# Performance work log

Hardware: AMD Instinct MI355X
Metric: run time of the kernel (lower is better)

## Reference

```python
import jax, jax.numpy as jnp
import numpy as np

D_MODEL = 1024
N_HEADS = 16
D_HEAD = D_MODEL // N_HEADS
EPS = 1e-6


def setup_inputs() -> dict:
    key = jax.random.key(0)
    ks = jax.random.split(key, 11)
    N, L, S = 4, 4096, 4096
    scale = 1.0 / np.sqrt(D_MODEL)
    inp = {
        "queries": jax.random.normal(ks[0], (N, L, D_MODEL), jnp.float32),
        "keys": jax.random.normal(ks[1], (N, S, D_MODEL), jnp.float32),
        "values": jax.random.normal(ks[2], (N, S, D_MODEL), jnp.float32),
        "Wq": jax.random.normal(ks[3], (D_MODEL, D_MODEL), jnp.float32) * scale,
        "bq": jnp.zeros((D_MODEL,), jnp.float32),
        "Wk": jax.random.normal(ks[4], (D_MODEL, D_MODEL), jnp.float32) * scale,
        "bk": jnp.zeros((D_MODEL,), jnp.float32),
        "Wv": jax.random.normal(ks[5], (D_MODEL, D_MODEL), jnp.float32) * scale,
        "bv": jnp.zeros((D_MODEL,), jnp.float32),
        "Wo": jax.random.normal(ks[6], (D_MODEL, D_MODEL), jnp.float32) * scale,
        "bo": jnp.zeros((D_MODEL,), jnp.float32),
    }
    return inp


def reference(queries, keys, values, Wq, bq, Wk, bk, Wv, bv, Wo, bo):
    N, L, _ = queries.shape
    S = keys.shape[1]
    H, Dh = N_HEADS, D_HEAD
    # projections (torch Linear: x @ W.T + b)
    q = (queries @ Wq.T + bq).reshape(N, L, H, Dh)
    k = (keys @ Wk.T + bk).reshape(N, S, H, Dh)
    v = (values @ Wv.T + bv).reshape(N, S, H, Dh)
    # elu+1 feature map
    Q = jax.nn.elu(q) + 1.0
    K = jax.nn.elu(k) + 1.0
    # KV summary: [N,H,Dv,Dh]
    KV = jnp.einsum('nshd,nshm->nhmd', K, v)
    # normalizer: [N,L,H]
    Z = 1.0 / (jnp.einsum('nlhd,nhd->nlh', Q, K.sum(axis=1)) + EPS)
    # output per head: [N,L,H,Dv]
    V = jnp.einsum('nlhd,nhmd,nlh->nlhm', Q, KV, Z)
    out = V.reshape(N, L, H * Dh) @ Wo.T + bo
    return out
```

## Files before the change

kernel.cpp:

```cpp
#include <hip/hip_runtime.h>
#include <hip/hip_bf16.h>

typedef __attribute__((ext_vector_type(8))) short short8;
typedef __attribute__((ext_vector_type(4))) short short4v;
typedef __attribute__((ext_vector_type(4))) float f32x4;

#define MFMA16(a, b, c) __builtin_amdgcn_mfma_f32_16x16x32_bf16(a, b, c, 0, 0, 0)

__device__ __forceinline__ unsigned short f2bf(float f) {
    unsigned int u = __float_as_uint(f);
    unsigned int r = u + 0x7fffu + ((u >> 16) & 1u);
    return (unsigned short)(r >> 16);
}
__device__ __forceinline__ float bf2f(unsigned short h) {
    return __uint_as_float(((unsigned int)h) << 16);
}
__device__ __forceinline__ unsigned int pk2(float lo, float hi) {
    return (unsigned int)f2bf(lo) | ((unsigned int)f2bf(hi) << 16);
}
__device__ __forceinline__ unsigned int cvtpk(float lo, float hi) {
    unsigned int r;
    asm("v_cvt_pk_bf16_f32 %0, %1, %2" : "=v"(r) : "v"(lo), "v"(hi));
    return r;
}

__device__ __forceinline__ void async16(const void* g, void* l) {
    __builtin_amdgcn_global_load_lds(
        (const __attribute__((address_space(1))) unsigned int*)g,
        (__attribute__((address_space(3))) unsigned int*)l, 16, 0, 0);
}

#define S_BARRIER() asm volatile("s_barrier" ::: "memory")
#define SCHED_FENCE() __builtin_amdgcn_sched_barrier(0)

__global__ __launch_bounds__(256) void cvt4_kernel(const float* __restrict__ w0,
                                                   const float* __restrict__ w1,
                                                   const float* __restrict__ w2,
                                                   const float* __restrict__ w3,
                                                   unsigned short* __restrict__ o0,
                                                   unsigned short* __restrict__ o1,
                                                   unsigned short* __restrict__ o2,
                                                   unsigned short* __restrict__ o3) {
    int wsel = blockIdx.x >> 7;
    int lb = blockIdx.x & 127;
    const float* in = wsel == 0 ? w0 : wsel == 1 ? w1 : wsel == 2 ? w2 : w3;
    unsigned short* out = wsel == 0 ? o0 : wsel == 1 ? o1 : wsel == 2 ? o2 : o3;
    for (int i = lb * 256 + threadIdx.x; i < 131072; i += 32768) {
        float4 v0 = reinterpret_cast<const float4*>(in)[2 * i];
        float4 v1 = reinterpret_cast<const float4*>(in)[2 * i + 1];
        uint4 p;
        p.x = pk2(v0.x, v0.y); p.y = pk2(v0.z, v0.w);
        p.z = pk2(v1.x, v1.y); p.w = pk2(v1.z, v1.w);
        reinterpret_cast<uint4*>(out)[i] = p;
    }
}

__device__ __forceinline__ void gemm_f32a(const float* __restrict__ A,
                                          const unsigned short* __restrict__ B,
                                          const float* __restrict__ bias,
                                          void* __restrict__ out,
                                          int mode, char* lds, int bid) {
    const int tid = threadIdx.x;
    const int lane = tid & 63, wid = tid >> 6;
    const int wr = wid >> 2, wc = wid & 3;
    const int lr = lane & 15, lg = lane >> 4;

    const int swz = (bid & 7) * 32 + (bid >> 3);
    const int bm = swz >> 2, bn = swz & 3;
    const long row0 = (long)bm * 256;
    const long col0 = (long)bn * 256;

    const float* srcA[4];
#pragma unroll
    for (int g = 0; g < 4; ++g) {
        int s = g * 512 + tid;
        int pr = s >> 3;
        int dc = (s & 7) ^ (pr & 7);
        srcA[g] = A + (row0 + pr) * 1024 + dc * 4;
    }
    const unsigned short* srcB[2];
#pragma unroll
    for (int g = 0; g < 2; ++g) {
        int s = g * 512 + tid;
        int pr = s >> 3;
        int dc = (s & 7) ^ (pr & 7);
        srcB[g] = B + (col0 + pr + 128 * (dc >> 2)) * 1024 + (dc & 3) * 8;
    }
    const int dst = tid * 16;

#define STAGE_A(BUF, KT) do {                                                   \
        async16(srcA[0] + (KT) * 32, (BUF) + dst);                              \
        async16(srcA[1] + (KT) * 32, (BUF) + 8192 + dst);                       \
        async16(srcA[2] + (KT) * 32, (BUF) + 16384 + dst);                      \
        async16(srcA[3] + (KT) * 32, (BUF) + 24576 + dst); } while (0)
#define STAGE_B(BUF, KT) do {                                                   \
        async16(srcB[0] + (KT) * 32, (BUF) + 32768 + dst);                      \
        async16(srcB[1] + (KT) * 32, (BUF) + 40960 + dst); } while (0)

    int offA[8];
#pragma unroll
    for (int m = 0; m < 8; ++m)
        offA[m] = (wr * 128 + m * 16 + lr) * 128 + (((2 * lg) ^ (lr & 7)) << 4);
    int offB[4];
#pragma unroll
    for (int n = 0; n < 4; ++n)
        offB[n] = 32768 + ((wc & 1) * 64 + n * 16 + lr) * 128 +
                  ((((wc >> 1) * 4 + lg) ^ (lr & 7)) << 4);

    f32x4 acc[8][4] = {};

    char* p0 = lds;
    char* p1 = lds + 49152;
    char* p2 = lds + 98304;

    STAGE_A(p0, 0); STAGE_B(p0, 0);
    STAGE_A(p1, 1); STAGE_B(p1, 1);
    asm volatile("s_waitcnt vmcnt(6)" ::: "memory");
    SCHED_FENCE();
    S_BARRIER();

#pragma unroll 1
    for (int kt = 0; kt < 32; ++kt) {
        short8 b[4];
        {
            float4 a0[4], a1[4];
#pragma unroll
            for (int m = 0; m < 4; ++m) {
                a0[m] = *(const float4*)(p0 + offA[m]);
                a1[m] = *(const float4*)(p0 + (offA[m] ^ 16));
            }
#pragma unroll
            for (int n = 0; n < 4; ++n) b[n] = *(const short8*)(p0 + offB[n]);
            SCHED_FENCE();
            if (kt < 30) STAGE_A(p2, kt + 2);
            asm volatile("s_waitcnt lgkmcnt(0)" ::: "memory");
            SCHED_FENCE();
            short8 af[4];
#pragma unroll
            for (int m = 0; m < 4; ++m) {
                union { unsigned int u[4]; short8 s; } cv;
                cv.u[0] = cvtpk(a0[m].x, a0[m].y);
                cv.u[1] = cvtpk(a0[m].z, a0[m].w);
                cv.u[2] = cvtpk(a1[m].x, a1[m].y);
                cv.u[3] = cvtpk(a1[m].z, a1[m].w);
                af[m] = cv.s;
            }
            __builtin_amdgcn_s_setprio(1);
#pragma unroll
            for (int m = 0; m < 4; ++m)
#pragma unroll
                for (int n = 0; n < 4; ++n)
                    acc[m][n] = MFMA16(af[m], b[n], acc[m][n]);
            __builtin_amdgcn_s_setprio(0);
            SCHED_FENCE();
            S_BARRIER();
        }
        {
            float4 a0[4], a1[4];
#pragma unroll
            for (int m = 0; m < 4; ++m) {
                a0[m] = *(const float4*)(p0 + offA[4 + m]);
                a1[m] = *(const float4*)(p0 + (offA[4 + m] ^ 16));
            }
            SCHED_FENCE();
            if (kt < 30) STAGE_B(p2, kt + 2);
            if (kt < 30) {
                asm volatile("s_waitcnt vmcnt(6)" ::: "memory");
            } else {
                asm volatile("s_waitcnt vmcnt(0)" ::: "memory");
            }
            SCHED_FENCE();
            asm volatile("s_waitcnt lgkmcnt(0)" ::: "memory");
            SCHED_FENCE();
            short8 af[4];
#pragma unroll
            for (int m = 0; m < 4; ++m) {
                union { unsigned int u[4]; short8 s; } cv;
                cv.u[0] = cvtpk(a0[m].x, a0[m].y);
                cv.u[1] = cvtpk(a0[m].z, a0[m].w);
                cv.u[2] = cvtpk(a1[m].x, a1[m].y);
                cv.u[3] = cvtpk(a1[m].z, a1[m].w);
                af[m] = cv.s;
            }
            __builtin_amdgcn_s_setprio(1);
#pragma unroll
            for (int m = 0; m < 4; ++m)
#pragma unroll
                for (int n = 0; n < 4; ++n)
                    acc[4 + m][n] = MFMA16(af[m], b[n], acc[4 + m][n]);
            __builtin_amdgcn_s_setprio(0);
            SCHED_FENCE();
            S_BARRIER();
        }
        char* t_ = p0; p0 = p1; p1 = p2; p2 = t_;
    }
#undef STAGE_A
#undef STAGE_B

    const int r4 = lg * 4;
    if (mode == 0) {
        char* ep = lds + wid * 4608;
#pragma unroll
        for (int m = 0; m < 8; ++m) {
#pragma unroll
            for (int n = 0; n < 4; ++n) {
                float bcol = bias[col0 + wc * 64 + n * 16 + lr];
#pragma unroll
                for (int j = 0; j < 4; ++j) {
                    float v = acc[m][n][j] + bcol;
                    v = v > 0.f ? v + 1.f : __expf(v);
                    *(float*)(ep + (((lg * 4 + j) * 68) + n * 16 + lr) * 4) = v;
                }
            }
            asm volatile("s_waitcnt lgkmcnt(0)" ::: "memory");
            SCHED_FENCE();
            long R0b = row0 + wr * 128 + m * 16;
            unsigned short* O = (unsigned short*)out;
#pragma unroll
            for (int i = 0; i < 2; ++i) {
                int r = i * 8 + (lane >> 3), c8 = (lane & 7) * 8;
                float4 u0 = *(const float4*)(ep + (r * 68 + c8) * 4);
                float4 u1 = *(const float4*)(ep + (r * 68 + c8 + 4) * 4);
                uint4 w;
                w.x = pk2(u0.x, u0.y); w.y = pk2(u0.z, u0.w);
                w.z = pk2(u1.x, u1.y); w.w = pk2(u1.z, u1.w);
                *(uint4*)(O + (R0b + r) * 1024 + col0 + wc * 64 + c8) = w;
            }
            asm volatile("s_waitcnt lgkmcnt(0)" ::: "memory");
            SCHED_FENCE();
        }
    } else {
#pragma unroll
        for (int m = 0; m < 8; ++m) {
#pragma unroll
            for (int n = 0; n < 4; ++n) {
                long col = col0 + wc * 64 + n * 16 + lr;
                float bcol = bias[col];
                long R0 = row0 + wr * 128 + m * 16 + r4;
                unsigned short* O = (unsigned short*)out;
                long nb = R0 >> 12;
                long s = R0 & 4095;
                short4v pack;
#pragma unroll
                for (int j = 0; j < 4; ++j) {
                    float v = acc[m][n][j] + bcol;
                    if (mode == 1) v = v > 0.f ? v + 1.f : __expf(v);
                    pack[j] = (short)f2bf(v);
                }
                *(short4v*)(O + ((nb << 10) + col) * 4096 + s) = pack;
            }
        }
    }
}

__device__ __forceinline__ void gemm_body(const unsigned short* __restrict__ A,
                                          const unsigned short* __restrict__ B,
                                          const float* __restrict__ bias,
                                          float* __restrict__ out,
                                          char* lds, int bid) {
    const int tid = threadIdx.x;
    const int lane = tid & 63, wid = tid >> 6;
    const int wr = wid >> 2, wc = wid & 3;
    const int lr = lane & 15, lg = lane >> 4;

    const int swz = (bid & 7) * 32 + (bid >> 3);
    const int bm = swz >> 2, bn = swz & 3;
    const long row0 = (long)bm * 256;
    const long col0 = (long)bn * 256;

    const unsigned short* srcA[2];
    const unsigned short* srcB[2];
    int dstOff[2];
#pragma unroll
    for (int g = 0; g < 2; ++g) {
        int s = g * 512 + tid;
        int pr = s >> 3;
        int dc = (s & 7) ^ (pr & 7);
        srcA[g] = A + (row0 + (pr & 63) + 128 * (pr >> 6)) * 1024 + dc * 8;
        srcB[g] = B + (col0 + pr) * 1024 + dc * 8;
        dstOff[g] = s * 16;
    }

#define STG_AQ(BB, Q, KT) do {                                                  \
        async16(srcA[0] + (Q) * 65536 + (KT) * 64,                              \
                lds + (BB) * 65536 + (Q) * 16384 + dstOff[0]);                  \
        async16(srcA[1] + (Q) * 65536 + (KT) * 64,                              \
                lds + (BB) * 65536 + (Q) * 16384 + dstOff[1]); } while (0)
#define STG_BH(BB, H, KT) do {                                                  \
        async16(srcB[0] + (H) * 131072 + (KT) * 64,                             \
                lds + (BB) * 65536 + 32768 + (H) * 16384 + dstOff[0]);          \
        async16(srcB[1] + (H) * 131072 + (KT) * 64,                             \
                lds + (BB) * 65536 + 32768 + (H) * 16384 + dstOff[1]); } while (0)

    const int ch0 = ((lg ^ (lr & 7)) << 4);
    const int ch1 = (((4 + lg) ^ (lr & 7)) << 4);
    const int aB0 = (64 * wr + lr) * 128 + ch0;
    const int aB1 = (64 * wr + lr) * 128 + ch1;
    const int bB0 = 32768 + (wc >> 1) * 16384 + ((wc & 1) * 64 + lr) * 128 + ch0;
    const int bB1 = 32768 + (wc >> 1) * 16384 + ((wc & 1) * 64 + lr) * 128 + ch1;

    f32x4 acc[8][4] = {};
    short8 b0[4], b1[4];

#define GATE4() do { asm volatile("s_waitcnt vmcnt(4)" ::: "memory"); SCHED_FENCE(); } while (0)
#define GATE0() do { asm volatile("s_waitcnt vmcnt(0)" ::: "memory"); SCHED_FENCE(); } while (0)
#define MFMA_BLOCK(MB, BV) do {                                                 \
        S_BARRIER();                                                            \
        asm volatile("s_waitcnt lgkmcnt(0)" ::: "memory");                      \
        SCHED_FENCE();                                                          \
        __builtin_amdgcn_s_setprio(1);                                          \
        _Pragma("unroll") for (int m = 0; m < 4; ++m)                           \
            _Pragma("unroll") for (int n = 0; n < 4; ++n)                       \
                acc[(MB) + m][n] = MFMA16(a[m], BV[n], acc[(MB) + m][n]);       \
        __builtin_amdgcn_s_setprio(0);                                          \
        SCHED_FENCE();                                                          \
        S_BARRIER(); } while (0)
#define LOAD_A(BUFB, ABASE, Q) do {                                             \
        _Pragma("unroll") for (int m = 0; m < 4; ++m)                           \
            a[m] = *(const short8*)(lds + (BUFB) + (Q) * 16384 + (ABASE) + m * 2048); } while (0)
#define LOAD_B(BUFB, BBASE, BV) do {                                            \
        _Pragma("unroll") for (int n = 0; n < 4; ++n)                           \
            BV[n] = *(const short8*)(lds + (BUFB) + (BBASE) + n * 2048); } while (0)

    STG_AQ(0, 0, 0); STG_BH(0, 0, 0); STG_BH(0, 1, 0); STG_AQ(0, 1, 0);
    STG_AQ(1, 0, 1); STG_BH(1, 0, 1);
    GATE4();
    S_BARRIER();

#pragma unroll 1
    for (int t = 0; t < 7; ++t) {
        const int ktA = 2 * t + 1, ktB = 2 * t + 2, ktC = 2 * t + 3;
        { short8 a[4]; LOAD_B(0, bB0, b0); LOAD_A(0, aB0, 0); STG_BH(1, 1, ktA); MFMA_BLOCK(0, b0); }
        { short8 a[4]; LOAD_B(0, bB1, b1); LOAD_A(0, aB1, 0); STG_AQ(1, 1, ktA); MFMA_BLOCK(0, b1); }
        { short8 a[4]; LOAD_A(0, aB0, 1); STG_AQ(0, 0, ktB); MFMA_BLOCK(4, b0); }
        { short8 a[4]; LOAD_A(0, aB1, 1); STG_BH(0, 0, ktB); GATE4(); MFMA_BLOCK(4, b1); }
        { short8 a[4]; LOAD_B(65536, bB0, b0); LOAD_A(65536, aB0, 0); STG_BH(0, 1, ktB); MFMA_BLOCK(0, b0); }
        { short8 a[4]; LOAD_B(65536, bB1, b1); LOAD_A(65536, aB1, 0); STG_AQ(0, 1, ktB); MFMA_BLOCK(0, b1); }
        { short8 a[4]; LOAD_A(65536, aB0, 1); STG_AQ(1, 0, ktC); MFMA_BLOCK(4, b0); }
        { short8 a[4]; LOAD_A(65536, aB1, 1); STG_BH(1, 0, ktC); GATE4(); MFMA_BLOCK(4, b1); }
    }
    {
        { short8 a[4]; LOAD_B(0, bB0, b0); LOAD_A(0, aB0, 0); STG_BH(1, 1, 15); MFMA_BLOCK(0, b0); }
        { short8 a[4]; LOAD_B(0, bB1, b1); LOAD_A(0, aB1, 0); STG_AQ(1, 1, 15); MFMA_BLOCK(0, b1); }
        { short8 a[4]; LOAD_A(0, aB0, 1); MFMA_BLOCK(4, b0); }
        { short8 a[4]; LOAD_A(0, aB1, 1); GATE0(); MFMA_BLOCK(4, b1); }
        { short8 a[4]; LOAD_B(65536, bB0, b0); LOAD_A(65536, aB0, 0); MFMA_BLOCK(0, b0); }
        { short8 a[4]; LOAD_B(65536, bB1, b1); LOAD_A(65536, aB1, 0); MFMA_BLOCK(0, b1); }
        { short8 a[4]; LOAD_A(65536, aB0, 1); MFMA_BLOCK(4, b0); }
        { short8 a[4]; LOAD_A(65536, aB1, 1); MFMA_BLOCK(4, b1); }
    }
#undef STG_AQ
#undef STG_BH
#undef GATE4
#undef GATE0
#undef MFMA_BLOCK
#undef LOAD_A
#undef LOAD_B

    {
        char* ep = lds + wid * 4608;
#pragma unroll
        for (int m = 0; m < 8; ++m) {
#pragma unroll
            for (int n = 0; n < 4; ++n) {
                float bcol = bias[col0 + wc * 64 + n * 16 + lr];
#pragma unroll
                for (int j = 0; j < 4; ++j)
                    *(float*)(ep + (((lg * 4 + j) * 68) + n * 16 + lr) * 4) = acc[m][n][j] + bcol;
            }
            asm volatile("s_waitcnt lgkmcnt(0)" ::: "memory");
            SCHED_FENCE();
            long R0b = row0 + wr * 128 + m * 16;
#pragma unroll
            for (int i = 0; i < 4; ++i) {
                int r = i * 4 + (lane >> 4), c4 = (lane & 15) * 4;
                float4 u = *(const float4*)(ep + (r * 68 + c4) * 4);
                *(float4*)(out + (R0b + r) * 1024 + col0 + wc * 64 + c4) = u;
            }
            asm volatile("s_waitcnt lgkmcnt(0)" ::: "memory");
            SCHED_FENCE();
        }
    }
}

__global__ __launch_bounds__(512, 1) void proj_gemm(const float* __restrict__ q,
                                                    const float* __restrict__ k,
                                                    const float* __restrict__ v,
                                                    const unsigned short* __restrict__ Wqb,
                                                    const unsigned short* __restrict__ Wkb,
                                                    const unsigned short* __restrict__ Wvb,
                                                    const float* __restrict__ bq,
                                                    const float* __restrict__ bk,
                                                    const float* __restrict__ bv,
                                                    unsigned short* __restrict__ Qm,
                                                    unsigned short* __restrict__ Kt,
                                                    unsigned short* __restrict__ vT) {
    __shared__ __align__(16) char lds[147456];
    int seg = blockIdx.x >> 8;
    int bid = blockIdx.x & 255;
    const float* A = seg == 0 ? q : seg == 1 ? k : v;
    const unsigned short* B = seg == 0 ? Wqb : seg == 1 ? Wkb : Wvb;
    const float* bias = seg == 0 ? bq : seg == 1 ? bk : bv;
    void* out = seg == 0 ? (void*)Qm : seg == 1 ? (void*)Kt : (void*)vT;
    gemm_f32a(A, B, bias, out, seg, lds, bid);
}

__global__ __launch_bounds__(512, 1) void out_gemm(const unsigned short* __restrict__ Vbuf,
                                                   const unsigned short* __restrict__ Wob,
                                                   const float* __restrict__ bo,
                                                   float* __restrict__ out) {
    __shared__ __align__(16) char lds[131072];
    gemm_body(Vbuf, Wob, bo, out, lds, blockIdx.x);
}

__global__ __launch_bounds__(256) void kv_kernel(const unsigned short* __restrict__ Kt,
                                                 const unsigned short* __restrict__ vT,
                                                 float* __restrict__ KV,
                                                 float* __restrict__ Ksum) {
    int b = blockIdx.x;
    int sc = b & 7, h = (b >> 3) & 15, n = b >> 7;
    const int tid = threadIdx.x, lane = tid & 63, wave = tid >> 6;
    long base = ((long)(n * 1024 + h * 64)) * 4096 + sc * 512;
    const unsigned short* Kp = Kt + base;
    const unsigned short* Vp = vT + base;
    const int lr = lane & 15, lk = (lane >> 4) * 8;

    f32x4 acc[4] = {};
    float ksa[4] = {0.f, 0.f, 0.f, 0.f};
    for (int s0 = 0; s0 < 512; s0 += 32) {
        short8 a = *(const short8*)(Vp + (long)(wave * 16 + lr) * 4096 + s0 + lk);
#pragma unroll
        for (int d4 = 0; d4 < 4; ++d4) {
            short8 bb = *(const short8*)(Kp + (long)(d4 * 16 + lr) * 4096 + s0 + lk);
            acc[d4] = MFMA16(a, bb, acc[d4]);
            if (wave == 0) {
                float t = 0.f;
#pragma unroll
                for (int e = 0; e < 8; ++e) t += bf2f((unsigned short)bb[e]);
                ksa[d4] += t;
            }
        }
    }
    float* KVb = KV + (long)(n * 16 + h) * 4096;
#pragma unroll
    for (int d4 = 0; d4 < 4; ++d4)
#pragma unroll
        for (int j = 0; j < 4; ++j) {
            int m = wave * 16 + (lane >> 4) * 4 + j;
            int d = d4 * 16 + lr;
            atomicAdd(KVb + m * 64 + d, acc[d4][j]);
        }
    if (wave == 0) {
#pragma unroll
        for (int d4 = 0; d4 < 4; ++d4) {
            float t = ksa[d4];
            t += __shfl_xor(t, 16, 64);
            t += __shfl_xor(t, 32, 64);
            if (lane < 16) atomicAdd(Ksum + n * 1024 + h * 64 + d4 * 16 + lane, t);
        }
    }
}

__global__ __launch_bounds__(256) void attn_kernel(const unsigned short* __restrict__ Qm,
                                                   const float* __restrict__ KV,
                                                   const float* __restrict__ Ksum,
                                                   unsigned short* __restrict__ Vbuf) {
    __shared__ unsigned short Qs[128 * 64];
    __shared__ unsigned short KVs[64 * 64];
    __shared__ float zin[128];
    __shared__ float ks[64];
    int b = blockIdx.x;
    int lc = b & 31, h = (b >> 5) & 15, n = b >> 9;
    int tid = threadIdx.x, lane = tid & 63, wave = tid >> 6;
    long l0 = (long)n * 4096 + lc * 128;

    const unsigned short* Qg = Qm + (l0 + (tid >> 3)) * 1024 + h * 64 + (tid & 7) * 8;
    char* QsB = (char*)Qs + (wave << 10);
#pragma unroll
    for (int it = 0; it < 4; ++it)
        async16(Qg + (long)it * 32 * 1024, QsB + it * 4096);

    const float* kvp = KV + (long)(n * 16 + h) * 4096;
    for (int i = tid * 4; i < 4096; i += 1024) {
        float4 v = *reinterpret_cast<const float4*>(kvp + i);
        short4v p;
        p[0] = (short)f2bf(v.x); p[1] = (short)f2bf(v.y);
        p[2] = (short)f2bf(v.z); p[3] = (short)f2bf(v.w);
        *(short4v*)(KVs + i) = p;
    }
    if (tid < 64) ks[tid] = Ksum[n * 1024 + h * 64 + tid];
    __syncthreads();

    {
        int row = tid >> 1, half = tid & 1;
        float den = 0.f;
        const unsigned short* qrow = Qs + row * 64 + half * 32;
#pragma unroll
        for (int d = 0; d < 32; ++d) den += bf2f(qrow[d]) * ks[half * 32 + d];
        den += __shfl_xor(den, 1, 64);
        if (half == 0) zin[row] = 1.0f / (den + 1e-6f);
    }
    __syncthreads();

    const int lr = lane & 15, lk = (lane >> 4) * 8;
    f32x4 acc[2][4] = {};
#pragma unroll
    for (int kk = 0; kk < 2; ++kk) {
        short8 a0 = *(const short8*)(Qs + (wave * 32 + lr) * 64 + kk * 32 + lk);
        short8 a1 = *(const short8*)(Qs + (wave * 32 + 16 + lr) * 64 + kk * 32 + lk);
#pragma unroll
        for (int nn = 0; nn < 4; ++nn) {
            short8 bb = *(const short8*)(KVs + (nn * 16 + lr) * 64 + kk * 32 + lk);
            acc[0][nn] = MFMA16(a0, bb, acc[0][nn]);
            acc[1][nn] = MFMA16(a1, bb, acc[1][nn]);
        }
    }

    {
        char* ep = (char*)Qs + wave * 4096;
#pragma unroll
        for (int mi = 0; mi < 2; ++mi) {
#pragma unroll
            for (int nn = 0; nn < 4; ++nn)
#pragma unroll
                for (int j = 0; j < 4; ++j) {
                    int rloc = (lane >> 4) * 4 + j;
                    float v = acc[mi][nn][j] * zin[wave * 32 + mi * 16 + rloc];
                    *(float*)(ep + (rloc * 64 + nn * 16 + lr) * 4) = v;
                }
            asm volatile("s_waitcnt lgkmcnt(0)" ::: "memory");
            SCHED_FENCE();
#pragma unroll
            for (int i = 0; i < 2; ++i) {
                int r = i * 8 + (lane >> 3), c8 = (lane & 7) * 8;
                float4 u0 = *(const float4*)(ep + (r * 64 + c8) * 4);
                float4 u1 = *(const float4*)(ep + (r * 64 + c8 + 4) * 4);
                uint4 w;
                w.x = pk2(u0.x, u0.y); w.y = pk2(u0.z, u0.w);
                w.z = pk2(u1.x, u1.y); w.w = pk2(u1.z, u1.w);
                *(uint4*)(Vbuf + (l0 + wave * 32 + mi * 16 + r) * 1024 + h * 64 + c8) = w;
            }
            asm volatile("s_waitcnt lgkmcnt(0)" ::: "memory");
            SCHED_FENCE();
        }
    }
}

extern "C" void kernel_launch(void* const* d_in, const int* in_sizes, int n_in,
                              void* d_out, int out_size, void* d_ws, size_t ws_size,
                              hipStream_t stream) {
    const float* queries = (const float*)d_in[0];
    const float* keys    = (const float*)d_in[1];
    const float* values  = (const float*)d_in[2];
    const float* Wq = (const float*)d_in[3];
    const float* bq = (const float*)d_in[4];
    const float* Wk = (const float*)d_in[5];
    const float* bk = (const float*)d_in[6];
    const float* Wv = (const float*)d_in[7];
    const float* bv = (const float*)d_in[8];
    const float* Wo = (const float*)d_in[9];
    const float* bo = (const float*)d_in[10];
    float* out = (float*)d_out;

    char* ws = (char*)d_ws;
    const size_t SZ = (size_t)16384 * 1024 * 2;
    const size_t WSZ = (size_t)1024 * 1024 * 2;
    unsigned short* Wqb = (unsigned short*)(ws);
    unsigned short* Wkb = (unsigned short*)(ws + WSZ);
    unsigned short* Wvb = (unsigned short*)(ws + 2 * WSZ);
    unsigned short* Wob = (unsigned short*)(ws + 3 * WSZ);
    unsigned short* Qm   = (unsigned short*)(ws + 4 * WSZ);
    unsigned short* Kt   = (unsigned short*)(ws + 4 * WSZ + SZ);
    unsigned short* vT   = (unsigned short*)(ws + 4 * WSZ + 2 * SZ);
    unsigned short* Vbuf = (unsigned short*)(ws + 4 * WSZ + 3 * SZ);
    float* KVf = (float*)(ws + 4 * WSZ + 4 * SZ);
    float* Ksf = (float*)(ws + 4 * WSZ + 4 * SZ + 1048576);

    hipMemsetAsync(KVf, 0, 1048576 + 16384, stream);

    cvt4_kernel<<<512, 256, 0, stream>>>(Wq, Wk, Wv, Wo, Wqb, Wkb, Wvb, Wob);

    proj_gemm<<<768, 512, 0, stream>>>(queries, keys, values, Wqb, Wkb, Wvb,
                                       bq, bk, bv, Qm, Kt, vT);

    kv_kernel<<<512, 256, 0, stream>>>(Kt, vT, KVf, Ksf);
    attn_kernel<<<2048, 256, 0, stream>>>(Qm, KVf, Ksf, Vbuf);

    out_gemm<<<256, 512, 0, stream>>>(Vbuf, Wob, bo, out);
}
```

Baseline: 233.3 us.

## Double waves per block in projection GEMM and drop mid-iteration barrier

Result: slower. 238.9 us (+2.4%).

```diff
diff --git a/kernel.cpp b/kernel.cpp
--- a/kernel.cpp
+++ b/kernel.cpp
@@ -70,52 +70,45 @@
     const long row0 = (long)bm * 256;
     const long col0 = (long)bn * 256;
 
-    const float* srcA[4];
-#pragma unroll
-    for (int g = 0; g < 4; ++g) {
-        int s = g * 512 + tid;
+    const float* srcA[2];
+#pragma unroll
+    for (int g = 0; g < 2; ++g) {
+        int s = g * 1024 + tid;
         int pr = s >> 3;
         int dc = (s & 7) ^ (pr & 7);
         srcA[g] = A + (row0 + pr) * 1024 + dc * 4;
     }
-    const unsigned short* srcB[2];
-#pragma unroll
-    for (int g = 0; g < 2; ++g) {
-        int s = g * 512 + tid;
-        int pr = s >> 3;
-        int dc = (s & 7) ^ (pr & 7);
-        srcB[g] = B + (col0 + pr + 128 * (dc >> 2)) * 1024 + (dc & 3) * 8;
+    const unsigned short* srcB;
+    {
+        int pr = tid >> 3;
+        int dc = (tid & 7) ^ (pr & 7);
+        srcB = B + (col0 + pr + 128 * (dc >> 2)) * 1024 + (dc & 3) * 8;
     }
     const int dst = tid * 16;
 
-#define STAGE_A(BUF, KT) do {                                                   \
+#define STAGE(BUF, KT) do {                                                     \
         async16(srcA[0] + (KT) * 32, (BUF) + dst);                              \
-        async16(srcA[1] + (KT) * 32, (BUF) + 8192 + dst);                       \
-        async16(srcA[2] + (KT) * 32, (BUF) + 16384 + dst);                      \
-        async16(srcA[3] + (KT) * 32, (BUF) + 24576 + dst); } while (0)
-#define STAGE_B(BUF, KT) do {                                                   \
-        async16(srcB[0] + (KT) * 32, (BUF) + 32768 + dst);                      \
-        async16(srcB[1] + (KT) * 32, (BUF) + 40960 + dst); } while (0)
-
-    int offA[8];
-#pragma unroll
-    for (int m = 0; m < 8; ++m)
-        offA[m] = (wr * 128 + m * 16 + lr) * 128 + (((2 * lg) ^ (lr & 7)) << 4);
+        async16(srcA[1] + (KT) * 32, (BUF) + 16384 + dst);                      \
+        async16(srcB + (KT) * 32, (BUF) + 32768 + dst); } while (0)
+
+    int offA[4];
+#pragma unroll
+    for (int m = 0; m < 4; ++m)
+        offA[m] = (wr * 64 + m * 16 + lr) * 128 + (((2 * lg) ^ (lr & 7)) << 4);
     int offB[4];
 #pragma unroll
     for (int n = 0; n < 4; ++n)
         offB[n] = 32768 + ((wc & 1) * 64 + n * 16 + lr) * 128 +
                   ((((wc >> 1) * 4 + lg) ^ (lr & 7)) << 4);
 
-    f32x4 acc[8][4] = {};
+    f32x4 acc[4][4] = {};
 
     char* p0 = lds;
     char* p1 = lds + 49152;
     char* p2 = lds + 98304;
 
-    STAGE_A(p0, 0); STAGE_B(p0, 0);
-    STAGE_A(p1, 1); STAGE_B(p1, 1);
-    asm volatile("s_waitcnt vmcnt(6)" ::: "memory");
+    STAGE(p0, 0); STAGE(p1, 1);
+    asm volatile("s_waitcnt vmcnt(3)" ::: "memory");
     SCHED_FENCE();
     S_BARRIER();
 
@@ -123,21 +116,21 @@
     for (int kt = 0; kt < 32; ++kt) {
         short8 b[4];
         {
-            float4 a0[4], a1[4];
-#pragma unroll
-            for (int m = 0; m < 4; ++m) {
+            float4 a0[2], a1[2];
+#pragma unroll
+            for (int n = 0; n < 4; ++n) b[n] = *(const short8*)(p0 + offB[n]);
+#pragma unroll
+            for (int m = 0; m < 2; ++m) {
                 a0[m] = *(const float4*)(p0 + offA[m]);
                 a1[m] = *(const float4*)(p0 + (offA[m] ^ 16));
             }
-#pragma unroll
-            for (int n = 0; n < 4; ++n) b[n] = *(const short8*)(p0 + offB[n]);
-            SCHED_FENCE();
-            if (kt < 30) STAGE_A(p2, kt + 2);
-            asm volatile("s_waitcnt lgkmcnt(0)" ::: "memory");
-            SCHED_FENCE();
-            short8 af[4];
-#pragma unroll
-            for (int m = 0; m < 4; ++m) {
+            SCHED_FENCE();
+            if (kt < 30) STAGE(p2, kt + 2);
+            asm volatile("s_waitcnt lgkmcnt(0)" ::: "memory");
+            SCHED_FENCE();
+            short8 af[2];
+#pragma unroll
+            for (int m = 0; m < 2; ++m) {
                 union { unsigned int u[4]; short8 s; } cv;
                 cv.u[0] = cvtpk(a0[m].x, a0[m].y);
                 cv.u[1] = cvtpk(a0[m].z, a0[m].w);
@@ -147,34 +140,25 @@
             }
             __builtin_amdgcn_s_setprio(1);
 #pragma unroll
-            for (int m = 0; m < 4; ++m)
+            for (int m = 0; m < 2; ++m)
 #pragma unroll
                 for (int n = 0; n < 4; ++n)
                     acc[m][n] = MFMA16(af[m], b[n], acc[m][n]);
             __builtin_amdgcn_s_setprio(0);
             SCHED_FENCE();
-            S_BARRIER();
         }
         {
-            float4 a0[4], a1[4];
-#pragma unroll
-            for (int m = 0; m < 4; ++m) {
-                a0[m] = *(const float4*)(p0 + offA[4 + m]);
-                a1[m] = *(const float4*)(p0 + (offA[4 + m] ^ 16));
-            }
-            SCHED_FENCE();
-            if (kt < 30) STAGE_B(p2, kt + 2);
-            if (kt < 30) {
-                asm volatile("s_waitcnt vmcnt(6)" ::: "memory");
-            } else {
-                asm volatile("s_waitcnt vmcnt(0)" ::: "memory");
-            }
-            SCHED_FENCE();
-            asm volatile("s_waitcnt lgkmcnt(0)" ::: "memory");
-            SCHED_FENCE();
-            short8 af[4];
-#pragma unroll
-            for (int m = 0; m < 4; ++m) {
+            float4 a0[2], a1[2];
+#pragma unroll
+            for (int m = 0; m < 2; ++m) {
+                a0[m] = *(const float4*)(p0 + offA[2 + m]);
+                a1[m] = *(const float4*)(p0 + (offA[2 + m] ^ 16));
+            }
+            asm volatile("s_waitcnt lgkmcnt(0)" ::: "memory");
+            SCHED_FENCE();
+            short8 af[2];
+#pragma unroll
+            for (int m = 0; m < 2; ++m) {
                 union { unsigned int u[4]; short8 s; } cv;
                 cv.u[0] = cvtpk(a0[m].x, a0[m].y);
                 cv.u[1] = cvtpk(a0[m].z, a0[m].w);
@@ -184,24 +168,29 @@
             }
             __builtin_amdgcn_s_setprio(1);
 #pragma unroll
-            for (int m = 0; m < 4; ++m)
+            for (int m = 0; m < 2; ++m)
 #pragma unroll
                 for (int n = 0; n < 4; ++n)
-                    acc[4 + m][n] = MFMA16(af[m], b[n], acc[4 + m][n]);
+                    acc[2 + m][n] = MFMA16(af[m], b[n], acc[2 + m][n]);
             __builtin_amdgcn_s_setprio(0);
             SCHED_FENCE();
+            if (kt < 30) {
+                asm volatile("s_waitcnt vmcnt(3)" ::: "memory");
+            } else {
+                asm volatile("s_waitcnt vmcnt(0)" ::: "memory");
+            }
+            SCHED_FENCE();
             S_BARRIER();
         }
         char* t_ = p0; p0 = p1; p1 = p2; p2 = t_;
     }
-#undef STAGE_A
-#undef STAGE_B
+#undef STAGE
 
     const int r4 = lg * 4;
     if (mode == 0) {
         char* ep = lds + wid * 4608;
 #pragma unroll
-        for (int m = 0; m < 8; ++m) {
+        for (int m = 0; m < 4; ++m) {
 #pragma unroll
             for (int n = 0; n < 4; ++n) {
                 float bcol = bias[col0 + wc * 64 + n * 16 + lr];
@@ -214,7 +203,7 @@
             }
             asm volatile("s_waitcnt lgkmcnt(0)" ::: "memory");
             SCHED_FENCE();
-            long R0b = row0 + wr * 128 + m * 16;
+            long R0b = row0 + wr * 64 + m * 16;
             unsigned short* O = (unsigned short*)out;
 #pragma unroll
             for (int i = 0; i < 2; ++i) {
@@ -231,12 +220,12 @@
         }
     } else {
 #pragma unroll
-        for (int m = 0; m < 8; ++m) {
+        for (int m = 0; m < 4; ++m) {
 #pragma unroll
             for (int n = 0; n < 4; ++n) {
                 long col = col0 + wc * 64 + n * 16 + lr;
                 float bcol = bias[col];
-                long R0 = row0 + wr * 128 + m * 16 + r4;
+                long R0 = row0 + wr * 64 + m * 16 + r4;
                 unsigned short* O = (unsigned short*)out;
                 long nb = R0 >> 12;
                 long s = R0 & 4095;
@@ -383,18 +372,18 @@
     }
 }
 
-__global__ __launch_bounds__(512, 1) void proj_gemm(const float* __restrict__ q,
-                                                    const float* __restrict__ k,
-                                                    const float* __restrict__ v,
-                                                    const unsigned short* __restrict__ Wqb,
-                                                    const unsigned short* __restrict__ Wkb,
-                                                    const unsigned short* __restrict__ Wvb,
-                                                    const float* __restrict__ bq,
-                                                    const float* __restrict__ bk,
-                                                    const float* __restrict__ bv,
-                                                    unsigned short* __restrict__ Qm,
-                                                    unsigned short* __restrict__ Kt,
-                                                    unsigned short* __restrict__ vT) {
+__global__ __launch_bounds__(1024) void proj_gemm(const float* __restrict__ q,
+                                                  const float* __restrict__ k,
+                                                  const float* __restrict__ v,
+                                                  const unsigned short* __restrict__ Wqb,
+                                                  const unsigned short* __restrict__ Wkb,
+                                                  const unsigned short* __restrict__ Wvb,
+                                                  const float* __restrict__ bq,
+                                                  const float* __restrict__ bk,
+                                                  const float* __restrict__ bv,
+                                                  unsigned short* __restrict__ Qm,
+                                                  unsigned short* __restrict__ Kt,
+                                                  unsigned short* __restrict__ vT) {
     __shared__ __align__(16) char lds[147456];
     int seg = blockIdx.x >> 8;
     int bid = blockIdx.x & 255;
@@ -580,8 +569,8 @@
 
     cvt4_kernel<<<512, 256, 0, stream>>>(Wq, Wk, Wv, Wo, Wqb, Wkb, Wvb, Wob);
 
-    proj_gemm<<<768, 512, 0, stream>>>(queries, keys, values, Wqb, Wkb, Wvb,
-                                       bq, bk, bv, Qm, Kt, vT);
+    proj_gemm<<<768, 1024, 0, stream>>>(queries, keys, values, Wqb, Wkb, Wvb,
+                                        bq, bk, bv, Qm, Kt, vT);
 
     kv_kernel<<<512, 256, 0, stream>>>(Kt, vT, KVf, Ksf);
     attn_kernel<<<2048, 256, 0, stream>>>(Qm, KVf, Ksf, Vbuf);
```
